# Kernel optimization log

Measured on AMD Instinct MI355X. Metric: run time of the kernel, lower is better.

## Reference

```python
import jax, jax.numpy as jnp
import numpy as np
from jax import lax

T, B, DIM, N = 1024, 64, 512, 64


def setup_inputs() -> dict:
    key = jax.random.key(0)
    k1, k2 = jax.random.split(key)
    x = jax.random.normal(k1, (T, B, DIM), dtype=jnp.float32)
    # xavier-uniform-like scale for fused projection [4n, dim]
    lim = float(np.sqrt(6.0 / (N + DIM)))
    W_kvqm = jax.random.uniform(k2, (4 * N, DIM), dtype=jnp.float32, minval=-lim, maxval=lim)
    return {
        "x": x,
        "S0": jnp.zeros((B, N, N), dtype=jnp.float32),
        "M0": jnp.zeros((B, N, N), dtype=jnp.float32),
        "W_kvqm": W_kvqm,
        "B_S": jnp.full((N, N), 2.0, dtype=jnp.float32),
        "B_M": jnp.full((N, N), 2.5, dtype=jnp.float32),
    }


def reference(x, S0, M0, W_kvqm, B_S, B_M):
    n = S0.shape[1]
    # fused projection for all timesteps: [T, B, 4n]
    proj = jnp.einsum('tbd,nd->tbn', x, W_kvqm)
    k_all, v_all, q_all, m_all = jnp.split(proj, 4, axis=-1)

    def step(carry, inp):
        S, M = carry
        k, v, q, m_vec = inp
        k_norm = k / (jnp.linalg.norm(k, axis=-1, keepdims=True) + 1e-6)
        m_norm = m_vec / (jnp.linalg.norm(m_vec, axis=-1, keepdims=True) + 1e-6)
        # S update gated by M
        M_k = jnp.einsum('bij,bj->bi', M, k_norm)
        G_S = jax.nn.sigmoid(M + jnp.einsum('bi,bj->bij', M_k, k_norm) + B_S)
        s_delta = v - jnp.einsum('bij,bj->bi', S, k_norm)
        S = G_S * S + jnp.einsum('bi,bj->bij', s_delta, k_norm)
        # M update gated by (new) S
        S_m = jnp.einsum('bij,bj->bi', S, m_norm)
        G_M = jax.nn.sigmoid(S + jnp.einsum('bi,bj->bij', S_m, m_norm) + B_M)
        m_delta = s_delta - jnp.einsum('bij,bj->bi', M, m_norm)
        M = G_M * M + jnp.einsum('bi,bj->bij', m_delta, m_norm)
        Sq = jnp.einsum('bij,bj->bi', S, q)
        out = Sq * jax.nn.silu(Sq)
        return (S, M), out

    (S, M), output = lax.scan(step, (S0, M0), (k_all, v_all, q_all, m_all))
    return output, S, M
```

## Files before the change

### kernel.cpp

```cpp
#include <hip/hip_runtime.h>
#include <cstddef>

#define T_STEPS 1024
#define BATCH   64
#define DIMK    512
#define NDIM    64
#define PROJW   256
#define STEPSTRIDE (BATCH * PROJW)

__device__ __forceinline__ float sigmoidf_(float x) {
    return 1.0f / (1.0f + __expf(-x));
}

template<int CTRL>
__device__ __forceinline__ float dpp_mov(float x) {
    return __int_as_float(__builtin_amdgcn_update_dpp(
        0, __float_as_int(x), CTRL, 0xF, 0xF, true));
}
__device__ __forceinline__ float rowsum16(float x) {
    x += dpp_mov<0x128>(x);
    x += dpp_mov<0x124>(x);
    x += dpp_mov<0x122>(x);
    x += dpp_mov<0x121>(x);
    return x;
}

__global__ __launch_bounds__(256) void proj_gemm(const float* __restrict__ X,
                                                 const float* __restrict__ W,
                                                 float* __restrict__ C) {
    __shared__ float As[16][132];
    __shared__ float Bs[16][132];
    const int tid  = threadIdx.x;
    const int row0 = blockIdx.x * 128;
    const int col0 = blockIdx.y * 128;
    const int tx4  = (tid & 15) << 2;
    const int ty4  = (tid >> 4) << 2;
    const int lm   = tid >> 2;
    const int lk   = (tid & 3) << 2;

    const float* Arow0 = X + (size_t)(row0 + lm)      * DIMK + lk;
    const float* Arow1 = X + (size_t)(row0 + lm + 64) * DIMK + lk;
    const float* Brow0 = W + (size_t)(col0 + lm)      * DIMK + lk;
    const float* Brow1 = W + (size_t)(col0 + lm + 64) * DIMK + lk;

    float acc[8][8] = {};
    float4 pa0, pa1, pb0, pb1;

    pa0 = *(const float4*)(Arow0);
    pa1 = *(const float4*)(Arow1);
    pb0 = *(const float4*)(Brow0);
    pb1 = *(const float4*)(Brow1);

    for (int tile = 0; tile < DIMK / 16; ++tile) {
        __syncthreads();
        As[lk+0][lm]    = pa0.x; As[lk+1][lm]    = pa0.y; As[lk+2][lm]    = pa0.z; As[lk+3][lm]    = pa0.w;
        As[lk+0][lm+64] = pa1.x; As[lk+1][lm+64] = pa1.y; As[lk+2][lm+64] = pa1.z; As[lk+3][lm+64] = pa1.w;
        Bs[lk+0][lm]    = pb0.x; Bs[lk+1][lm]    = pb0.y; Bs[lk+2][lm]    = pb0.z; Bs[lk+3][lm]    = pb0.w;
        Bs[lk+0][lm+64] = pb1.x; Bs[lk+1][lm+64] = pb1.y; Bs[lk+2][lm+64] = pb1.z; Bs[lk+3][lm+64] = pb1.w;
        __syncthreads();
        if (tile + 1 < DIMK / 16) {
            const int kb = (tile + 1) * 16;
            pa0 = *(const float4*)(Arow0 + kb);
            pa1 = *(const float4*)(Arow1 + kb);
            pb0 = *(const float4*)(Brow0 + kb);
            pb1 = *(const float4*)(Brow1 + kb);
        }
        #pragma unroll 8
        for (int k = 0; k < 16; ++k) {
            const float4 a0v = *(const float4*)&As[k][ty4];
            const float4 a1v = *(const float4*)&As[k][64 + ty4];
            const float4 b0v = *(const float4*)&Bs[k][tx4];
            const float4 b1v = *(const float4*)&Bs[k][64 + tx4];
            const float a[8]  = {a0v.x, a0v.y, a0v.z, a0v.w, a1v.x, a1v.y, a1v.z, a1v.w};
            const float bb[8] = {b0v.x, b0v.y, b0v.z, b0v.w, b1v.x, b1v.y, b1v.z, b1v.w};
            #pragma unroll
            for (int i2 = 0; i2 < 8; ++i2)
                #pragma unroll
                for (int j2 = 0; j2 < 8; ++j2)
                    acc[i2][j2] = fmaf(a[i2], bb[j2], acc[i2][j2]);
        }
    }

    #pragma unroll
    for (int h = 0; h < 2; ++h) {
        #pragma unroll
        for (int r = 0; r < 4; ++r) {
            const size_t R = (size_t)(row0 + h * 64 + ty4 + r) * PROJW + col0;
            float4 o0 = {acc[h*4+r][0], acc[h*4+r][1], acc[h*4+r][2], acc[h*4+r][3]};
            float4 o1 = {acc[h*4+r][4], acc[h*4+r][5], acc[h*4+r][6], acc[h*4+r][7]};
            *(float4*)&C[R + tx4]      = o0;
            *(float4*)&C[R + 64 + tx4] = o1;
        }
    }
}

__global__ __launch_bounds__(256) void normalize_km(float* __restrict__ proj) {
    const int p    = blockIdx.x * 4 + (threadIdx.x >> 6);
    const int lane = threadIdx.x & 63;
    float* base = proj + (size_t)p * PROJW;
    const float k = base[lane];
    const float m = base[192 + lane];
    float sk = k * k, sm = m * m;
    #pragma unroll
    for (int d = 1; d < 64; d <<= 1) {
        sk += __shfl_xor(sk, d);
        sm += __shfl_xor(sm, d);
    }
    base[lane]       = k / (sqrtf(sk) + 1e-6f);
    base[192 + lane] = m / (sqrtf(sm) + 1e-6f);
}

__global__ __launch_bounds__(256) void recur_kernel(const float* __restrict__ proj,
                                                    const float* __restrict__ S0,
                                                    const float* __restrict__ M0,
                                                    const float* __restrict__ BSmat,
                                                    const float* __restrict__ BMmat,
                                                    float* __restrict__ outp,
                                                    float* __restrict__ Sout,
                                                    float* __restrict__ Mout) {
    const int tid = threadIdx.x;
    const int b   = blockIdx.x & 63;
    const int rt  = blockIdx.x >> 6;
    const int rl  = tid >> 4;
    const int i   = (rt << 4) + rl;
    const int l16 = tid & 15;
    const int j0  = l16 << 2;

    float S[4], Mr[4], BSr[4], BMr[4];
    const size_t smoff = ((size_t)b * NDIM + i) * NDIM + j0;
    { float4 t4 = *(const float4*)&S0[smoff];                    S[0]=t4.x;  S[1]=t4.y;  S[2]=t4.z;  S[3]=t4.w;  }
    { float4 t4 = *(const float4*)&M0[smoff];                    Mr[0]=t4.x; Mr[1]=t4.y; Mr[2]=t4.z; Mr[3]=t4.w; }
    { float4 t4 = *(const float4*)&BSmat[(size_t)i * NDIM + j0]; BSr[0]=t4.x;BSr[1]=t4.y;BSr[2]=t4.z;BSr[3]=t4.w;}
    { float4 t4 = *(const float4*)&BMmat[(size_t)i * NDIM + j0]; BMr[0]=t4.x;BMr[1]=t4.y;BMr[2]=t4.z;BMr[3]=t4.w;}

    const float* pb = proj + (size_t)b * PROJW;

    auto step = [&](int t, float4 kn4, float4 q4, float4 mn4, float v_i) {
        const float kr[4] = {kn4.x, kn4.y, kn4.z, kn4.w};
        const float qr[4] = {q4.x,  q4.y,  q4.z,  q4.w};
        const float mr[4] = {mn4.x, mn4.y, mn4.z, mn4.w};

        float Mk = 0.f, Sk = 0.f, Mm = 0.f;
        #pragma unroll
        for (int c = 0; c < 4; ++c) {
            Mk = fmaf(Mr[c], kr[c], Mk);
            Sk = fmaf(S[c],  kr[c], Sk);
            Mm = fmaf(Mr[c], mr[c], Mm);
        }
        Mk = rowsum16(Mk); Sk = rowsum16(Sk); Mm = rowsum16(Mm);
        const float sd = v_i - Sk;

        #pragma unroll
        for (int c = 0; c < 4; ++c) {
            const float gs = sigmoidf_(fmaf(Mk, kr[c], Mr[c]) + BSr[c]);
            S[c] = fmaf(gs, S[c], sd * kr[c]);
        }
        float Sm = 0.f, Sq = 0.f;
        #pragma unroll
        for (int c = 0; c < 4; ++c) {
            Sm = fmaf(S[c], mr[c], Sm);
            Sq = fmaf(S[c], qr[c], Sq);
        }
        Sm = rowsum16(Sm); Sq = rowsum16(Sq);
        const float md = sd - Mm;

        #pragma unroll
        for (int c = 0; c < 4; ++c) {
            const float gm = sigmoidf_(fmaf(Sm, mr[c], S[c]) + BMr[c]);
            Mr[c] = fmaf(gm, Mr[c], md * mr[c]);
        }
        if (l16 == 0) {
            outp[(size_t)t * (BATCH * NDIM) + b * NDIM + i] = Sq * Sq * sigmoidf_(Sq);
        }
    };

#define DECL_SET(s) float4 kn##s, q##s, mn##s; float vi##s;
#define LOAD_SET(s, tt) { \
        const int t_ = ((tt) < T_STEPS) ? (tt) : (T_STEPS - 1); \
        const float* r_ = pb + (size_t)t_ * STEPSTRIDE; \
        kn##s = *(const float4*)(r_ + j0); \
        q##s  = *(const float4*)(r_ + 128 + j0); \
        mn##s = *(const float4*)(r_ + 192 + j0); \
        vi##s = r_[64 + i]; }

    DECL_SET(0) DECL_SET(1) DECL_SET(2) DECL_SET(3)
    LOAD_SET(0, 0) LOAD_SET(1, 1) LOAD_SET(2, 2) LOAD_SET(3, 3)

    for (int t = 0; t < T_STEPS; t += 4) {
        step(t + 0, kn0, q0, mn0, vi0); LOAD_SET(0, t + 4);
        step(t + 1, kn1, q1, mn1, vi1); LOAD_SET(1, t + 5);
        step(t + 2, kn2, q2, mn2, vi2); LOAD_SET(2, t + 6);
        step(t + 3, kn3, q3, mn3, vi3); LOAD_SET(3, t + 7);
    }
#undef DECL_SET
#undef LOAD_SET

    { float4 o = {S[0], S[1], S[2], S[3]};     *(float4*)&Sout[smoff] = o; }
    { float4 o = {Mr[0], Mr[1], Mr[2], Mr[3]}; *(float4*)&Mout[smoff] = o; }
}

extern "C" void kernel_launch(void* const* d_in, const int* in_sizes, int n_in,
                              void* d_out, int out_size, void* d_ws, size_t ws_size,
                              hipStream_t stream) {
    const float* x   = (const float*)d_in[0];
    const float* S0  = (const float*)d_in[1];
    const float* M0  = (const float*)d_in[2];
    const float* W   = (const float*)d_in[3];
    const float* BS  = (const float*)d_in[4];
    const float* BMb = (const float*)d_in[5];
    float* out = (float*)d_out;

    float* proj = (float*)d_ws;

    dim3 g1(512, 2), b1(256);
    proj_gemm<<<g1, b1, 0, stream>>>(x, W, proj);

    normalize_km<<<dim3(T_STEPS * BATCH / 4), dim3(256), 0, stream>>>(proj);

    float* Sout = out + (size_t)T_STEPS * BATCH * NDIM;
    float* Mout = Sout + (size_t)BATCH * NDIM * NDIM;
    recur_kernel<<<dim3(BATCH * 4), dim3(256), 0, stream>>>(proj, S0, M0, BS, BMb,
                                                            out, Sout, Mout);
}
```

Before: 865.8 us.

## Split recurrence rows across 32 lanes and double recurrence grid size

The recurrence kernel now assigns each row of S/M to 32 lanes holding 2 columns each, instead of 16 lanes holding 4, and launches twice as many blocks (8 row-groups per batch). This shortens per-thread serial work on the latency-bound time loop and spreads the 64x64 state over more CUs. The price is an extra cross-row shuffle in every reduction and more redundant loads of k/q/m per block. The sigmoid also switches to the hardware reciprocal approximation.

After: 734.5 us. -15.2%, faster.

```diff
diff --git a/kernel.cpp b/kernel.cpp
--- a/kernel.cpp
+++ b/kernel.cpp
@@ -9,7 +9,7 @@
 #define STEPSTRIDE (BATCH * PROJW)
 
 __device__ __forceinline__ float sigmoidf_(float x) {
-    return 1.0f / (1.0f + __expf(-x));
+    return __builtin_amdgcn_rcpf(1.0f + __expf(-x));
 }
 
 template<int CTRL>
@@ -17,11 +17,12 @@
     return __int_as_float(__builtin_amdgcn_update_dpp(
         0, __float_as_int(x), CTRL, 0xF, 0xF, true));
 }
-__device__ __forceinline__ float rowsum16(float x) {
+__device__ __forceinline__ float redrow32(float x) {
     x += dpp_mov<0x128>(x);
     x += dpp_mov<0x124>(x);
     x += dpp_mov<0x122>(x);
     x += dpp_mov<0x121>(x);
+    x += __shfl_xor(x, 16);
     return x;
 }
 
@@ -120,67 +121,57 @@
                                                     float* __restrict__ Mout) {
     const int tid = threadIdx.x;
     const int b   = blockIdx.x & 63;
-    const int rt  = blockIdx.x >> 6;
-    const int rl  = tid >> 4;
-    const int i   = (rt << 4) + rl;
-    const int l16 = tid & 15;
-    const int j0  = l16 << 2;
-
-    float S[4], Mr[4], BSr[4], BMr[4];
+    const int oct = blockIdx.x >> 6;
+    const int lr  = tid >> 5;
+    const int i   = (oct << 3) + lr;
+    const int l32 = tid & 31;
+    const int j0  = l32 << 1;
+
+    float S[2], Mr[2], BSr[2], BMr[2];
     const size_t smoff = ((size_t)b * NDIM + i) * NDIM + j0;
-    { float4 t4 = *(const float4*)&S0[smoff];                    S[0]=t4.x;  S[1]=t4.y;  S[2]=t4.z;  S[3]=t4.w;  }
-    { float4 t4 = *(const float4*)&M0[smoff];                    Mr[0]=t4.x; Mr[1]=t4.y; Mr[2]=t4.z; Mr[3]=t4.w; }
-    { float4 t4 = *(const float4*)&BSmat[(size_t)i * NDIM + j0]; BSr[0]=t4.x;BSr[1]=t4.y;BSr[2]=t4.z;BSr[3]=t4.w;}
-    { float4 t4 = *(const float4*)&BMmat[(size_t)i * NDIM + j0]; BMr[0]=t4.x;BMr[1]=t4.y;BMr[2]=t4.z;BMr[3]=t4.w;}
+    { float2 t2 = *(const float2*)&S0[smoff];                    S[0]=t2.x;  S[1]=t2.y;  }
+    { float2 t2 = *(const float2*)&M0[smoff];                    Mr[0]=t2.x; Mr[1]=t2.y; }
+    { float2 t2 = *(const float2*)&BSmat[(size_t)i * NDIM + j0]; BSr[0]=t2.x;BSr[1]=t2.y;}
+    { float2 t2 = *(const float2*)&BMmat[(size_t)i * NDIM + j0]; BMr[0]=t2.x;BMr[1]=t2.y;}
 
     const float* pb = proj + (size_t)b * PROJW;
 
-    auto step = [&](int t, float4 kn4, float4 q4, float4 mn4, float v_i) {
-        const float kr[4] = {kn4.x, kn4.y, kn4.z, kn4.w};
-        const float qr[4] = {q4.x,  q4.y,  q4.z,  q4.w};
-        const float mr[4] = {mn4.x, mn4.y, mn4.z, mn4.w};
-
-        float Mk = 0.f, Sk = 0.f, Mm = 0.f;
-        #pragma unroll
-        for (int c = 0; c < 4; ++c) {
-            Mk = fmaf(Mr[c], kr[c], Mk);
-            Sk = fmaf(S[c],  kr[c], Sk);
-            Mm = fmaf(Mr[c], mr[c], Mm);
-        }
-        Mk = rowsum16(Mk); Sk = rowsum16(Sk); Mm = rowsum16(Mm);
+    auto step = [&](int t, float2 kn2, float2 q2, float2 mn2, float v_i) {
+        float Mk = Mr[0] * kn2.x; Mk = fmaf(Mr[1], kn2.y, Mk);
+        float Sk = S[0]  * kn2.x; Sk = fmaf(S[1],  kn2.y, Sk);
+        float Mm = Mr[0] * mn2.x; Mm = fmaf(Mr[1], mn2.y, Mm);
+        Mk = redrow32(Mk); Sk = redrow32(Sk); Mm = redrow32(Mm);
         const float sd = v_i - Sk;
 
-        #pragma unroll
-        for (int c = 0; c < 4; ++c) {
-            const float gs = sigmoidf_(fmaf(Mk, kr[c], Mr[c]) + BSr[c]);
-            S[c] = fmaf(gs, S[c], sd * kr[c]);
-        }
-        float Sm = 0.f, Sq = 0.f;
-        #pragma unroll
-        for (int c = 0; c < 4; ++c) {
-            Sm = fmaf(S[c], mr[c], Sm);
-            Sq = fmaf(S[c], qr[c], Sq);
-        }
-        Sm = rowsum16(Sm); Sq = rowsum16(Sq);
+        {
+            const float g0 = sigmoidf_(fmaf(Mk, kn2.x, Mr[0]) + BSr[0]);
+            const float g1 = sigmoidf_(fmaf(Mk, kn2.y, Mr[1]) + BSr[1]);
+            S[0] = fmaf(g0, S[0], sd * kn2.x);
+            S[1] = fmaf(g1, S[1], sd * kn2.y);
+        }
+        float Sm = S[0] * mn2.x; Sm = fmaf(S[1], mn2.y, Sm);
+        float Sq = S[0] * q2.x;  Sq = fmaf(S[1], q2.y,  Sq);
+        Sm = redrow32(Sm); Sq = redrow32(Sq);
         const float md = sd - Mm;
 
-        #pragma unroll
-        for (int c = 0; c < 4; ++c) {
-            const float gm = sigmoidf_(fmaf(Sm, mr[c], S[c]) + BMr[c]);
-            Mr[c] = fmaf(gm, Mr[c], md * mr[c]);
-        }
-        if (l16 == 0) {
+        {
+            const float g0 = sigmoidf_(fmaf(Sm, mn2.x, S[0]) + BMr[0]);
+            const float g1 = sigmoidf_(fmaf(Sm, mn2.y, S[1]) + BMr[1]);
+            Mr[0] = fmaf(g0, Mr[0], md * mn2.x);
+            Mr[1] = fmaf(g1, Mr[1], md * mn2.y);
+        }
+        if (l32 == 0) {
             outp[(size_t)t * (BATCH * NDIM) + b * NDIM + i] = Sq * Sq * sigmoidf_(Sq);
         }
     };
 
-#define DECL_SET(s) float4 kn##s, q##s, mn##s; float vi##s;
+#define DECL_SET(s) float2 kn##s, q##s, mn##s; float vi##s;
 #define LOAD_SET(s, tt) { \
         const int t_ = ((tt) < T_STEPS) ? (tt) : (T_STEPS - 1); \
         const float* r_ = pb + (size_t)t_ * STEPSTRIDE; \
-        kn##s = *(const float4*)(r_ + j0); \
-        q##s  = *(const float4*)(r_ + 128 + j0); \
-        mn##s = *(const float4*)(r_ + 192 + j0); \
+        kn##s = *(const float2*)(r_ + j0); \
+        q##s  = *(const float2*)(r_ + 128 + j0); \
+        mn##s = *(const float2*)(r_ + 192 + j0); \
         vi##s = r_[64 + i]; }
 
     DECL_SET(0) DECL_SET(1) DECL_SET(2) DECL_SET(3)
@@ -195,8 +186,8 @@
 #undef DECL_SET
 #undef LOAD_SET
 
-    { float4 o = {S[0], S[1], S[2], S[3]};     *(float4*)&Sout[smoff] = o; }
-    { float4 o = {Mr[0], Mr[1], Mr[2], Mr[3]}; *(float4*)&Mout[smoff] = o; }
+    { float2 o = {S[0], S[1]};   *(float2*)&Sout[smoff] = o; }
+    { float2 o = {Mr[0], Mr[1]}; *(float2*)&Mout[smoff] = o; }
 }
 
 extern "C" void kernel_launch(void* const* d_in, const int* in_sizes, int n_in,
@@ -219,6 +210,6 @@
 
     float* Sout = out + (size_t)T_STEPS * BATCH * NDIM;
     float* Mout = Sout + (size_t)BATCH * NDIM * NDIM;
-    recur_kernel<<<dim3(BATCH * 4), dim3(256), 0, stream>>>(proj, S0, M0, BS, BMb,
+    recur_kernel<<<dim3(BATCH * 8), dim3(256), 0, stream>>>(proj, S0, M0, BS, BMb,
                                                             out, Sout, Mout);
 }
```
